# Performance work log

Measured on AMD Instinct MI355X. Metric: run time of the kernel, lower is better.

Reference implementation:

```python
import jax, jax.numpy as jnp
import numpy as np

EMBED = 32; HEADS = 4; HD = 8; FFN = 64; OBS = 64; CTX = 128; BATCH = 16
INIT_SCALE = 1.0 / np.sqrt(2.0 * 5.0)  # 1/sqrt(2*(3 spatial + 2 temporal))


def rmsnorm(x, w, eps=1e-6):
    return x / jnp.sqrt(jnp.mean(x * x, axis=-1, keepdims=True) + eps) * w


def rope_cache(T):
    theta = 1.0 / (10000.0 ** (jnp.arange(0, HD, 2, dtype=jnp.float32) / HD))
    freqs = jnp.arange(T, dtype=jnp.float32)[:, None] * theta[None, :]  # [T, HD//2]
    return jnp.cos(freqs), jnp.sin(freqs)


def apply_rope(x, cos, sin):
    half = x.shape[-1] // 2
    x1, x2 = x[..., :half], x[..., half:]
    c, s = cos[None, None], sin[None, None]  # broadcast over [B, H, T, HD//2]
    return jnp.concatenate([x1 * c - x2 * s, x2 * c + x1 * s], axis=-1)


def attn_block(x, Wq, Wk, Wv, Wo, Wg, Wval, Wout, norm4, qkn, cos=None, sin=None):
    B, S, W = x.shape
    h = rmsnorm(x, norm4[0])

    def proj(Wm):
        return jnp.einsum('bsw,dw->bsd', h, Wm).reshape(B, S, HEADS, HD).transpose(0, 2, 1, 3)

    q = rmsnorm(proj(Wq), qkn[0])
    k = rmsnorm(proj(Wk), qkn[1])
    v = proj(Wv)
    if cos is not None:
        q = apply_rope(q, cos, sin)
        k = apply_rope(k, cos, sin)
    scores = jnp.einsum('bhqd,bhkd->bhqk', q, k) / np.float32(np.sqrt(HD))
    o = jnp.einsum('bhqk,bhkd->bhqd', jax.nn.softmax(scores, axis=-1), v)
    o = o.transpose(0, 2, 1, 3).reshape(B, S, W)
    x = x + rmsnorm(jnp.einsum('bsw,dw->bsd', o, Wo), norm4[1])
    h2 = rmsnorm(x, norm4[2])
    ffn = jax.nn.silu(jnp.einsum('bsw,fw->bsf', h2, Wg)) * jnp.einsum('bsw,fw->bsf', h2, Wval)
    x = x + rmsnorm(jnp.einsum('bsf,wf->bsw', ffn, Wout), norm4[3])
    return x


def setup_inputs():
    key = jax.random.key(0)
    ks = iter(jax.random.split(key, 40))
    sd = 1.0 / np.sqrt(EMBED)
    inp = {
        'obs_seq': jax.random.normal(next(ks), (BATCH, CTX, OBS), jnp.float32),
        'W_val': jax.random.normal(next(ks), (EMBED, 1), jnp.float32),
        'b_val': jnp.zeros((EMBED,), jnp.float32),
        'input_norm_w': jnp.ones((EMBED,), jnp.float32),
        'dim_embed': jax.random.normal(next(ks), (OBS, EMBED), jnp.float32),
        'cls_tokens': jax.random.normal(next(ks), (3, EMBED), jnp.float32) * sd,
        'final_norm_w': jnp.ones((EMBED,), jnp.float32),
    }
    for pre, n in (('s', 3), ('t', 2)):
        inp[pre + '_Wq'] = jax.random.normal(next(ks), (n, EMBED, EMBED), jnp.float32) * sd
        inp[pre + '_Wk'] = jax.random.normal(next(ks), (n, EMBED, EMBED), jnp.float32) * sd
        inp[pre + '_Wv'] = jax.random.normal(next(ks), (n, EMBED, EMBED), jnp.float32) * sd
        inp[pre + '_Wo'] = jax.random.normal(next(ks), (n, EMBED, EMBED), jnp.float32) * (0.1 * INIT_SCALE * sd)
        inp[pre + '_Wg'] = jax.random.normal(next(ks), (n, FFN, EMBED), jnp.float32) * sd
        inp[pre + '_Wval'] = jax.random.normal(next(ks), (n, FFN, EMBED), jnp.float32) * sd
        inp[pre + '_Wout'] = jax.random.normal(next(ks), (n, EMBED, FFN), jnp.float32) * (INIT_SCALE / np.sqrt(FFN))
        inp[pre + '_norm4'] = jnp.ones((n, 4, EMBED), jnp.float32)
        inp[pre + '_qkn'] = jnp.ones((n, 2, HD), jnp.float32)
    return inp


def reference(obs_seq, W_val, b_val, input_norm_w, dim_embed, cls_tokens, final_norm_w,
              s_Wq, s_Wk, s_Wv, s_Wo, s_Wg, s_Wval, s_Wout, s_norm4, s_qkn,
              t_Wq, t_Wk, t_Wv, t_Wo, t_Wg, t_Wval, t_Wout, t_norm4, t_qkn):
    B, T, D = obs_seq.shape
    slots = D + 3
    # value_proj: Linear(1, EMBED) applied to each scalar feature
    tok = obs_seq[..., None] * W_val[:, 0] + b_val            # [B, T, D, EMBED]
    tok = tok + dim_embed[None, None]                          # dim id embedding
    cls = jnp.broadcast_to(cls_tokens[None, None], (B, T, 3, EMBED))
    tokens = rmsnorm(jnp.concatenate([tok, cls], axis=2), input_norm_w)  # [B,T,slots,EMBED]
    cos, sin = rope_cache(T)

    def spatial(tk, i):
        x = tk.reshape(B * T, slots, EMBED)
        x = attn_block(x, s_Wq[i], s_Wk[i], s_Wv[i], s_Wo[i], s_Wg[i], s_Wval[i], s_Wout[i], s_norm4[i], s_qkn[i])
        return x.reshape(B, T, slots, EMBED)

    def temporal(tk, i):
        x = tk.transpose(0, 2, 1, 3).reshape(B * slots, T, EMBED)
        x = attn_block(x, t_Wq[i], t_Wk[i], t_Wv[i], t_Wo[i], t_Wg[i], t_Wval[i], t_Wout[i], t_norm4[i], t_qkn[i], cos, sin)
        return x.reshape(B, slots, T, EMBED).transpose(0, 2, 1, 3)

    tokens = spatial(tokens, 0)
    tokens = temporal(tokens, 0)
    tokens = spatial(tokens, 1)
    tokens = temporal(tokens, 1)
    tokens = spatial(tokens, 2)
    tokens = rmsnorm(tokens, final_norm_w)
    last = tokens[:, -1]  # [B, slots, EMBED]
    return last[:, D], last[:, D + 1], last[:, D + 2]
```

## Files before the change

kernel.cpp:

```cpp
#include <hip/hip_runtime.h>

#define B_ 16
#define T_ 128
#define OBS_ 64
#define SLOTS_ 67
#define E_ 32
#define H_ 4
#define HD_ 8
#define FFN_ 64

typedef _Float16 h2 __attribute__((ext_vector_type(2)));
typedef _Float16 h4 __attribute__((ext_vector_type(4)));
typedef _Float16 h8 __attribute__((ext_vector_type(8)));
typedef __fp16 mh4 __attribute__((ext_vector_type(4)));
typedef __fp16 mh8 __attribute__((ext_vector_type(8)));
typedef float fx4 __attribute__((ext_vector_type(4)));
union H4u { h4 v; h2 h[2]; };

#define WBLK 10240
#define X16_BYTES (B_ * T_ * SLOTS_ * E_ * 2)
#define W16_BYTES (5 * WBLK * 2)
#define ROPE_OFF (X16_BYTES + W16_BYTES)
#define EMBED_BLOCKS ((B_ * T_ * SLOTS_ + 7) / 8)

__device__ __forceinline__ float red32(float v) {
  v += __shfl_xor(v, 16); v += __shfl_xor(v, 8); v += __shfl_xor(v, 4);
  v += __shfl_xor(v, 2);  v += __shfl_xor(v, 1);
  return v;
}
__device__ __forceinline__ float red8(float v) {
  v += __shfl_xor(v, 4); v += __shfl_xor(v, 2); v += __shfl_xor(v, 1);
  return v;
}
__device__ __forceinline__ float bfly16(float v) {
  v += __shfl_xor(v, 1); v += __shfl_xor(v, 2);
  v += __shfl_xor(v, 4); v += __shfl_xor(v, 8);
  return v;
}
__device__ __forceinline__ h2 pkrtz(float x, float y) {
  return __builtin_bit_cast(h2, __builtin_amdgcn_cvt_pkrtz(x, y));
}
__device__ __forceinline__ float rcp_(float x) { return __builtin_amdgcn_rcpf(x); }
__device__ __forceinline__ float rsq_(float x) { return __builtin_amdgcn_rsqf(x); }
__device__ __forceinline__ fx4 mfma16(h8 a, h8 b, fx4 c) {
  return __builtin_amdgcn_mfma_f32_16x16x32_f16(
      __builtin_bit_cast(mh8, a), __builtin_bit_cast(mh8, b), c, 0, 0, 0);
}
__device__ __forceinline__ fx4 mfma16k16(h4 a, h4 b, fx4 c) {
  return __builtin_amdgcn_mfma_f32_16x16x16f16(
      __builtin_bit_cast(mh4, a), __builtin_bit_cast(mh4, b), c, 0, 0, 0);
}

struct WPtrs {
  const float *sWq, *sWk, *sWv, *sWo, *sWg, *sWvl, *sWout;
  const float *tWq, *tWk, *tWv, *tWo, *tWg, *tWvl, *tWout;
};

#define CVT_BLOCKS 100

__global__ __launch_bounds__(256) void setup_kernel(
    WPtrs p, _Float16* __restrict__ dst,
    const float* __restrict__ obs, const float* __restrict__ Wval,
    const float* __restrict__ bval, const float* __restrict__ innw,
    const float* __restrict__ dimemb, const float* __restrict__ cls,
    float2* __restrict__ rope, _Float16* __restrict__ X) {
  if (blockIdx.x < CVT_BLOCKS) {
    int i = blockIdx.x * 256 + threadIdx.x;
    const int total_pairs = 5 * WBLK / 2;
    if (i >= total_pairs) return;
    int blk = i / (WBLK / 2);
    int f = (i % (WBLK / 2)) * 2;
    bool sp = blk < 3;
    int bi = sp ? blk : blk - 3;
    const float* src;
    int o;
    if (f < 1024)      { src = (sp ? p.sWq : p.tWq) + bi * 1024;  o = f; }
    else if (f < 2048) { src = (sp ? p.sWk : p.tWk) + bi * 1024;  o = f - 1024; }
    else if (f < 3072) { src = (sp ? p.sWv : p.tWv) + bi * 1024;  o = f - 2048; }
    else if (f < 4096) { src = (sp ? p.sWo : p.tWo) + bi * 1024;  o = f - 3072; }
    else if (f < 6144) { src = (sp ? p.sWg : p.tWg) + bi * 2048;  o = f - 4096; }
    else if (f < 8192) { src = (sp ? p.sWvl : p.tWvl) + bi * 2048; o = f - 6144; }
    else               { src = (sp ? p.sWout : p.tWout) + bi * 2048; o = f - 8192; }
    ((h2*)dst)[i] = pkrtz(src[o], src[o + 1]);
  } else if (blockIdx.x < CVT_BLOCKS + EMBED_BLOCKS) {
    int tok = (blockIdx.x - CVT_BLOCKS) * 8 + (threadIdx.x >> 5);
    int e = threadIdx.x & 31;
    const int total = B_ * T_ * SLOTS_;
    if (tok >= total) return;
    int slot = tok % SLOTS_;
    int bt = tok / SLOTS_;
    float v;
    if (slot < OBS_) {
      float o = obs[bt * OBS_ + slot];
      v = o * Wval[e] + bval[e] + dimemb[slot * E_ + e];
    } else {
      v = cls[(slot - OBS_) * E_ + e];
    }
    float ss = red32(v * v);
    X[tok * E_ + e] = (_Float16)(v * rsq_(ss * (1.0f / E_) + 1e-6f) * innw[e]);
  } else {
    for (int i = threadIdx.x; i < T_ * 4; i += 256) {
      int pos = i >> 2, j = i & 3;
      float th = __builtin_amdgcn_exp2f(-(float)j * 3.3219280948873623f);
      float sv, cv;
      __sincosf((float)pos * th, &sv, &cv);
      rope[i] = make_float2(cv, sv);
    }
  }
}

template <int SV, int SP, bool TEMPORAL, bool LAST>
__device__ __forceinline__ void block_body(
    _Float16* __restrict__ X, const _Float16* __restrict__ W16,
    const float* __restrict__ norm4, const float* __restrict__ qkn,
    const float2* __restrict__ rope, const float* __restrict__ fnw,
    float* __restrict__ out, int bid) {
  constexpr int MT = SP / 16;
  constexpr int MTW = (MT + 3) / 4;
  constexpr int VSTRIDE = TEMPORAL ? 128 : 168;
  constexpr int VROWS = TEMPORAL ? 32 : 33;
  __shared__ __align__(16) _Float16 smem[SP * 96 + VROWS * VSTRIDE];
  _Float16* hb = smem;
  _Float16* qb = smem + SP * 32;
  _Float16* kb = smem + SP * 64;
  _Float16* vT = smem + SP * 96;
  _Float16* ffnb = qb;

  const int tid = threadIdx.x;
  const int l = tid & 63, wv = tid >> 6;
  const int lm = l & 15, lq = l >> 4, hd = l & 7;

  auto vt_idx = [](int d, int s) {
    if (TEMPORAL) return d * 128 + (((s & ~15) ^ ((d & 7) << 4)) | (s & 15));
    return d * VSTRIDE + s;
  };

  int base, stride;
  if (TEMPORAL) {
    int b = bid / SLOTS_;
    int slot = bid % SLOTS_;
    base = (b * T_ * SLOTS_ + slot) * E_;
    stride = SLOTS_ * E_;
  } else {
    base = bid * 2 * SLOTS_ * E_;
    stride = E_;
  }

  const float nw0a = norm4[lm],      nw0b = norm4[16 + lm];
  const float nw1a = norm4[32 + lm], nw1b = norm4[48 + lm];
  const float nw2a = norm4[64 + lm], nw2b = norm4[80 + lm];
  const float nw3a = norm4[96 + lm], nw3b = norm4[112 + lm];
  const fx4 fz = {0.f, 0.f, 0.f, 0.f};
  const float qw = qkn[hd], kw = qkn[8 + hd];
  const float qscale = 0.35355339059327373f * 1.4426950408889634f;

  float xr[MTW][4][2];
#pragma unroll
  for (int t = 0; t < MTW; t++) {
    int mt = wv + 4 * t;
    if (mt < MT) {
#pragma unroll
      for (int r = 0; r < 4; r++) {
        int s = mt * 16 + lq * 4 + r;
        bool ok = (SV == SP) || (s < SV);
        int off = base + s * stride;
        xr[t][r][0] = ok ? (float)X[off + lm] : 0.f;
        xr[t][r][1] = ok ? (float)X[off + 16 + lm] : 0.f;
      }
    }
  }
#pragma unroll
  for (int t = 0; t < MTW; t++) {
    int mt = wv + 4 * t;
    if (mt < MT) {
#pragma unroll
      for (int r = 0; r < 4; r++) {
        int s = mt * 16 + lq * 4 + r;
        float p = bfly16(xr[t][r][0] * xr[t][r][0] + xr[t][r][1] * xr[t][r][1]);
        float inv = rsq_(p * (1.0f / E_) + 1e-6f);
        if (SV == SP || s < SV) {
          hb[s * 32 + lm] = (_Float16)(xr[t][r][0] * inv * nw0a);
          hb[s * 32 + 16 + lm] = (_Float16)(xr[t][r][1] * inv * nw0b);
        }
      }
    }
  }
  __syncthreads();

  for (int u = wv; u < MT * 2; u += 4) {
    const int mt = u >> 1, nt = u & 1;
    h8 aH = *(const h8*)(hb + (mt * 16 + lm) * 32 + lq * 8);
    float rc[4], rs[4];
    if (TEMPORAL) {
#pragma unroll
      for (int r = 0; r < 4; r++) {
        float2 cs = rope[(mt * 16 + lq * 4 + r) * 4 + (hd & 3)];
        rc[r] = cs.x; rs[r] = cs.y;
      }
    }
    const int d = nt * 16 + lm;
    h8 bq = *(const h8*)(W16 + (nt * 16 + lm) * 32 + lq * 8);
    h8 bk = *(const h8*)(W16 + 1024 + (nt * 16 + lm) * 32 + lq * 8);
    h8 bv = *(const h8*)(W16 + 2048 + (nt * 16 + lm) * 32 + lq * 8);
    fx4 aq = mfma16(aH, bq, fz);
    fx4 ak = mfma16(aH, bk, fz);
    fx4 av = mfma16(aH, bv, fz);
#pragma unroll
    for (int r = 0; r < 4; r++) {
      int s = mt * 16 + lq * 4 + r;
      float q1 = aq[r], k1 = ak[r];
      float qv = q1 * rsq_(red8(q1 * q1) * 0.125f + 1e-6f) * qw;
      float kv = k1 * rsq_(red8(k1 * k1) * 0.125f + 1e-6f) * kw;
      if (TEMPORAL) {
        float qp = __shfl_xor(qv, 4);
        float kp = __shfl_xor(kv, 4);
        qv = (hd < 4) ? (qv * rc[r] - qp * rs[r]) : (qv * rc[r] + qp * rs[r]);
        kv = (hd < 4) ? (kv * rc[r] - kp * rs[r]) : (kv * rc[r] + kp * rs[r]);
      }
      if (SV == SP || s < SV) {
        qb[s * 32 + d] = (_Float16)(qv * qscale);
        kb[s * 32 + d] = (_Float16)kv;
      }
    }
    const int s0 = mt * 16 + lq * 4;
    const int va = vt_idx(d, s0);
    if (SV == SP || s0 + 1 < SV) *(h2*)(vT + va) = pkrtz(av[0], av[1]);
    if (SV == SP || s0 + 3 < SV) *(h2*)(vT + va + 2) = pkrtz(av[2], av[3]);
  }
  if (!TEMPORAL) {
    for (int idx = tid; idx < 32 * 13; idx += 256) {
      int d = idx / 13, c = 2 * SLOTS_ + 2 * (idx % 13);
      *(h2*)(vT + d * VSTRIDE + c) = pkrtz(0.f, 0.f);
    }
    for (int idx = tid; idx < VSTRIDE / 2; idx += 256) {
      *(h2*)(vT + 32 * VSTRIDE + 2 * idx) = pkrtz(1.f, 1.f);
    }
  }
  __syncthreads();

  {
    const int h = wv;
    const h8 z8 = {};
    const h4 ones4 = {(_Float16)1.f, (_Float16)1.f, (_Float16)1.f, (_Float16)1.f};
    const bool vlane = (lm < 8);
    const int dv = h * 8 + (lm & 7);
    const int vrow = (!TEMPORAL && !vlane) ? 32 : dv;
    for (int mt = 0; mt < MT; mt++) {
      h8 bQ = *(const h8*)(qb + (mt * 16 + lm) * 32 + lq * 8);
      bQ = (lq == h) ? bQ : z8;
      const int q = mt * 16 + lm;
      fx4 oaccT = fz;

      auto ktile = [&](int kt, int mode) {
        h8 aK = *(const h8*)(kb + (kt * 16 + lm) * 32 + lq * 8);
        fx4 sc = mfma16(aK, bQ, fz);
        float ev[4];
#pragma unroll
        for (int r = 0; r < 4; r++) {
          float x = __builtin_amdgcn_exp2f(sc[r]);
          int kidx = kt * 16 + lq * 4 + r;
          if (mode == 1) x = (kidx < SLOTS_) ? x : 0.f;
          else if (mode == 2) x = (kidx >= SLOTS_) ? x : 0.f;
          else if (mode == 3) x = (kidx < 2 * SLOTS_) ? x : 0.f;
          else if (mode == 4) {
            bool ok = (kidx < 2 * SLOTS_) && ((kidx < SLOTS_) == (q < SLOTS_));
            x = ok ? x : 0.f;
          }
          ev[r] = x;
        }
        H4u pT;
        pT.h[0] = pkrtz(ev[0], ev[1]);
        pT.h[1] = pkrtz(ev[2], ev[3]);
        h4 aV = *(const h4*)(vT + vt_idx(vrow, kt * 16 + lq * 4));
        if (TEMPORAL) aV = vlane ? aV : ones4;
        oaccT = mfma16k16(aV, pT.v, oaccT);
      };

      if (TEMPORAL) {
#pragma unroll
        for (int kt = 0; kt < SP / 16; kt++) ktile(kt, 0);
      } else if (mt <= 3) {
#pragma unroll
        for (int kt = 0; kt < 4; kt++) ktile(kt, 0);
        ktile(4, 1);
      } else if (mt == 4) {
#pragma unroll
        for (int kt = 0; kt < MT; kt++) ktile(kt, 4);
      } else {
        ktile(4, 2);
#pragma unroll
        for (int kt = 5; kt < 8; kt++) ktile(kt, 0);
        ktile(8, 3);
      }

      float lsum = __shfl_xor(oaccT[0], 32);
      float inv = rcp_(lsum);
      if (lq < 2 && (SV == SP || q < SV)) {
        H4u ov;
        ov.h[0] = pkrtz(oaccT[0] * inv, oaccT[1] * inv);
        ov.h[1] = pkrtz(oaccT[2] * inv, oaccT[3] * inv);
        *(h4*)(hb + q * 32 + h * 8 + lq * 4) = ov.v;
      }
    }
  }
  __syncthreads();

#pragma unroll
  for (int t = 0; t < MTW; t++) {
    int mt = wv + 4 * t;
    if (mt < MT) {
      h8 aO = *(const h8*)(hb + (mt * 16 + lm) * 32 + lq * 8);
      h8 b0 = *(const h8*)(W16 + 3072 + lm * 32 + lq * 8);
      h8 b1 = *(const h8*)(W16 + 3072 + (16 + lm) * 32 + lq * 8);
      fx4 a0 = mfma16(aO, b0, fz);
      fx4 a1 = mfma16(aO, b1, fz);
#pragma unroll
      for (int r = 0; r < 4; r++) {
        int s = mt * 16 + lq * 4 + r;
        float p = bfly16(a0[r] * a0[r] + a1[r] * a1[r]);
        float inv = rsq_(p * (1.0f / E_) + 1e-6f);
        xr[t][r][0] += a0[r] * inv * nw1a;
        xr[t][r][1] += a1[r] * inv * nw1b;
        float q2 = bfly16(xr[t][r][0] * xr[t][r][0] + xr[t][r][1] * xr[t][r][1]);
        float inv2 = rsq_(q2 * (1.0f / E_) + 1e-6f);
        if (SV == SP || s < SV) {
          hb[s * 32 + lm] = (_Float16)(xr[t][r][0] * inv2 * nw2a);
          hb[s * 32 + 16 + lm] = (_Float16)(xr[t][r][1] * inv2 * nw2b);
        }
      }
    }
  }
  __syncthreads();

  for (int u = wv; u < MT * 4; u += 4) {
    const int mt = u >> 2, nt = u & 3;
    h8 aH2 = *(const h8*)(hb + (mt * 16 + lm) * 32 + lq * 8);
    h8 bg = *(const h8*)(W16 + 4096 + (nt * 16 + lm) * 32 + lq * 8);
    h8 bl = *(const h8*)(W16 + 6144 + (nt * 16 + lm) * 32 + lq * 8);
    fx4 g = mfma16(aH2, bg, fz);
    fx4 vvv = mfma16(aH2, bl, fz);
#pragma unroll
    for (int r = 0; r < 4; r++) {
      int s = mt * 16 + lq * 4 + r;
      if (SV == SP || s < SV) {
        float gg = g[r];
        float sg = gg * rcp_(1.0f + __builtin_amdgcn_exp2f(gg * -1.4426950408889634f));
        ffnb[s * 64 + nt * 16 + lm] = (_Float16)(sg * vvv[r]);
      }
    }
  }
  __syncthreads();

#pragma unroll
  for (int t = 0; t < MTW; t++) {
    int mt = wv + 4 * t;
    if (mt < MT) {
      const _Float16* fr = ffnb + (mt * 16 + lm) * 64;
      h8 a0 = *(const h8*)(fr + lq * 8);
      h8 a1 = *(const h8*)(fr + 32 + lq * 8);
      h8 b00 = *(const h8*)(W16 + 8192 + lm * 64 + lq * 8);
      h8 b01 = *(const h8*)(W16 + 8192 + lm * 64 + 32 + lq * 8);
      h8 b10 = *(const h8*)(W16 + 8192 + (16 + lm) * 64 + lq * 8);
      h8 b11 = *(const h8*)(W16 + 8192 + (16 + lm) * 64 + 32 + lq * 8);
      fx4 o0 = mfma16(a1, b01, mfma16(a0, b00, fz));
      fx4 o1 = mfma16(a1, b11, mfma16(a0, b10, fz));
#pragma unroll
      for (int r = 0; r < 4; r++) {
        int s = mt * 16 + lq * 4 + r;
        float p = bfly16(o0[r] * o0[r] + o1[r] * o1[r]);
        float inv = rsq_(p * (1.0f / E_) + 1e-6f);
        xr[t][r][0] += o0[r] * inv * nw3a;
        xr[t][r][1] += o1[r] * inv * nw3b;
        if (SV == SP || s < SV) {
          int off = base + s * stride;
          X[off + lm] = (_Float16)xr[t][r][0];
          X[off + 16 + lm] = (_Float16)xr[t][r][1];
        }
      }
      if (LAST && mt == MT - 1 && (bid & (T_ / 2 - 1)) == (T_ / 2 - 1)) {
        const int b = bid / (T_ / 2);
#pragma unroll
        for (int r = 0; r < 4; r++) {
          int s = mt * 16 + lq * 4 + r;
          int j = s - (SLOTS_ + OBS_);
          float p2 = bfly16(xr[t][r][0] * xr[t][r][0] + xr[t][r][1] * xr[t][r][1]);
          if (j >= 0 && j < 3) {
            float inv2 = rsq_(p2 * (1.0f / E_) + 1e-6f);
            out[j * (B_ * E_) + b * E_ + lm] = xr[t][r][0] * inv2 * fnw[lm];
            out[j * (B_ * E_) + b * E_ + 16 + lm] = xr[t][r][1] * inv2 * fnw[16 + lm];
          }
        }
      }
    }
  }
}

__global__ __launch_bounds__(256, 4) void attn_spatial_kernel(
    _Float16* __restrict__ X, const _Float16* __restrict__ W16,
    const float* __restrict__ norm4, const float* __restrict__ qkn) {
  block_body<2 * SLOTS_, 144, false, false>(X, W16, norm4, qkn, nullptr,
                                            nullptr, nullptr, blockIdx.x);
}

__global__ __launch_bounds__(256, 4) void attn_spatial_last_kernel(
    _Float16* __restrict__ X, const _Float16* __restrict__ W16,
    const float* __restrict__ norm4, const float* __restrict__ qkn,
    const float* __restrict__ fnw, float* __restrict__ out) {
  block_body<2 * SLOTS_, 144, false, true>(X, W16, norm4, qkn, nullptr,
                                           fnw, out, blockIdx.x);
}

__global__ __launch_bounds__(256, 5) void attn_temporal_kernel(
    _Float16* __restrict__ X, const _Float16* __restrict__ W16,
    const float* __restrict__ norm4, const float* __restrict__ qkn,
    const float2* __restrict__ rope) {
  block_body<T_, 128, true, false>(X, W16, norm4, qkn, rope,
                                   nullptr, nullptr, blockIdx.x);
}

extern "C" void kernel_launch(void* const* d_in, const int* in_sizes, int n_in,
                              void* d_out, int out_size, void* d_ws, size_t ws_size,
                              hipStream_t stream) {
  (void)in_sizes; (void)n_in; (void)out_size; (void)ws_size;
  const float* obs          = (const float*)d_in[0];
  const float* W_val        = (const float*)d_in[1];
  const float* b_val        = (const float*)d_in[2];
  const float* input_norm_w = (const float*)d_in[3];
  const float* dim_embed    = (const float*)d_in[4];
  const float* cls_tokens   = (const float*)d_in[5];
  const float* final_norm_w = (const float*)d_in[6];
  const float* s_n4   = (const float*)d_in[14];
  const float* s_qkn  = (const float*)d_in[15];
  const float* t_n4   = (const float*)d_in[23];
  const float* t_qkn  = (const float*)d_in[24];

  _Float16* X = (_Float16*)d_ws;
  _Float16* W16 = (_Float16*)((char*)d_ws + X16_BYTES);
  float2* rope = (float2*)((char*)d_ws + ROPE_OFF);
  float* out = (float*)d_out;

  WPtrs wp;
  wp.sWq   = (const float*)d_in[7];
  wp.sWk   = (const float*)d_in[8];
  wp.sWv   = (const float*)d_in[9];
  wp.sWo   = (const float*)d_in[10];
  wp.sWg   = (const float*)d_in[11];
  wp.sWvl  = (const float*)d_in[12];
  wp.sWout = (const float*)d_in[13];
  wp.tWq   = (const float*)d_in[16];
  wp.tWk   = (const float*)d_in[17];
  wp.tWv   = (const float*)d_in[18];
  wp.tWo   = (const float*)d_in[19];
  wp.tWg   = (const float*)d_in[20];
  wp.tWvl  = (const float*)d_in[21];
  wp.tWout = (const float*)d_in[22];

  setup_kernel<<<CVT_BLOCKS + EMBED_BLOCKS + 1, 256, 0, stream>>>(
      wp, W16, obs, W_val, b_val, input_norm_w, dim_embed, cls_tokens, rope, X);

  const int N4 = 4 * E_;
  const int QN = 2 * HD_;

#define SPATIAL(i)                                                     \
  attn_spatial_kernel<<<B_ * T_ / 2, 256, 0, stream>>>(                \
      X, W16 + (i)*WBLK, s_n4 + (i)*N4, s_qkn + (i)*QN)
#define TEMPORAL(i)                                                    \
  attn_temporal_kernel<<<B_ * SLOTS_, 256, 0, stream>>>(               \
      X, W16 + (3 + (i)) * WBLK, t_n4 + (i)*N4, t_qkn + (i)*QN, rope)

  SPATIAL(0);
  TEMPORAL(0);
  SPATIAL(1);
  TEMPORAL(1);
  attn_spatial_last_kernel<<<B_ * T_ / 2, 256, 0, stream>>>(
      X, W16 + 2 * WBLK, s_n4 + 2 * N4, s_qkn + 2 * QN, final_norm_w, out);

#undef SPATIAL
#undef TEMPORAL
}
```

Before: 310.4 us.

## Swizzle LDS buffers, pair query tiles in attention, batch embed tokens per block

Adds XOR-swizzled shared-memory indexing for the hb/qb/kb (32-wide) and ffnb (64-wide) buffers to reduce LDS bank conflicts on the h8 row loads. Restructures the attention loop so each K tile load and V load serves two query tiles at once, with two independent MFMA chains for more instruction-level parallelism. Makes the setup embedding blocks process 64 tokens each instead of 8. The costs are higher register pressure from the paired accumulators and extra index arithmetic; EMBED_BLOCKS now relies on the token count dividing evenly by 64.

```diff
diff --git a/kernel.cpp b/kernel.cpp
--- a/kernel.cpp
+++ b/kernel.cpp
@@ -21,7 +21,7 @@
 #define X16_BYTES (B_ * T_ * SLOTS_ * E_ * 2)
 #define W16_BYTES (5 * WBLK * 2)
 #define ROPE_OFF (X16_BYTES + W16_BYTES)
-#define EMBED_BLOCKS ((B_ * T_ * SLOTS_ + 7) / 8)
+#define EMBED_BLOCKS (B_ * T_ * SLOTS_ / 64)
 
 __device__ __forceinline__ float red32(float v) {
   v += __shfl_xor(v, 16); v += __shfl_xor(v, 8); v += __shfl_xor(v, 4);
@@ -49,6 +49,13 @@
 __device__ __forceinline__ fx4 mfma16k16(h4 a, h4 b, fx4 c) {
   return __builtin_amdgcn_mfma_f32_16x16x16f16(
       __builtin_bit_cast(mh4, a), __builtin_bit_cast(mh4, b), c, 0, 0, 0);
+}
+
+__device__ __forceinline__ int sw32(int row, int col) {
+  return row * 32 + (col ^ (((row >> 1) & 3) << 3));
+}
+__device__ __forceinline__ int sw64(int row, int col) {
+  return row * 64 + (col ^ ((row & 7) << 3));
 }
 
 struct WPtrs {
@@ -83,21 +90,23 @@
     else               { src = (sp ? p.sWout : p.tWout) + bi * 2048; o = f - 8192; }
     ((h2*)dst)[i] = pkrtz(src[o], src[o + 1]);
   } else if (blockIdx.x < CVT_BLOCKS + EMBED_BLOCKS) {
-    int tok = (blockIdx.x - CVT_BLOCKS) * 8 + (threadIdx.x >> 5);
+    int t0 = (blockIdx.x - CVT_BLOCKS) * 64 + (threadIdx.x >> 5);
     int e = threadIdx.x & 31;
-    const int total = B_ * T_ * SLOTS_;
-    if (tok >= total) return;
-    int slot = tok % SLOTS_;
-    int bt = tok / SLOTS_;
-    float v;
-    if (slot < OBS_) {
-      float o = obs[bt * OBS_ + slot];
-      v = o * Wval[e] + bval[e] + dimemb[slot * E_ + e];
-    } else {
-      v = cls[(slot - OBS_) * E_ + e];
-    }
-    float ss = red32(v * v);
-    X[tok * E_ + e] = (_Float16)(v * rsq_(ss * (1.0f / E_) + 1e-6f) * innw[e]);
+#pragma unroll
+    for (int i = 0; i < 8; i++) {
+      int tok = t0 + i * 8;
+      int slot = tok % SLOTS_;
+      int bt = tok / SLOTS_;
+      float v;
+      if (slot < OBS_) {
+        float o = obs[bt * OBS_ + slot];
+        v = o * Wval[e] + bval[e] + dimemb[slot * E_ + e];
+      } else {
+        v = cls[(slot - OBS_) * E_ + e];
+      }
+      float ss = red32(v * v);
+      X[tok * E_ + e] = (_Float16)(v * rsq_(ss * (1.0f / E_) + 1e-6f) * innw[e]);
+    }
   } else {
     for (int i = threadIdx.x; i < T_ * 4; i += 256) {
       int pos = i >> 2, j = i & 3;
@@ -179,8 +188,8 @@
         float p = bfly16(xr[t][r][0] * xr[t][r][0] + xr[t][r][1] * xr[t][r][1]);
         float inv = rsq_(p * (1.0f / E_) + 1e-6f);
         if (SV == SP || s < SV) {
-          hb[s * 32 + lm] = (_Float16)(xr[t][r][0] * inv * nw0a);
-          hb[s * 32 + 16 + lm] = (_Float16)(xr[t][r][1] * inv * nw0b);
+          hb[sw32(s, lm)] = (_Float16)(xr[t][r][0] * inv * nw0a);
+          hb[sw32(s, 16 + lm)] = (_Float16)(xr[t][r][1] * inv * nw0b);
         }
       }
     }
@@ -189,7 +198,7 @@
 
   for (int u = wv; u < MT * 2; u += 4) {
     const int mt = u >> 1, nt = u & 1;
-    h8 aH = *(const h8*)(hb + (mt * 16 + lm) * 32 + lq * 8);
+    h8 aH = *(const h8*)(hb + sw32(mt * 16 + lm, lq * 8));
     float rc[4], rs[4];
     if (TEMPORAL) {
 #pragma unroll
@@ -218,8 +227,8 @@
         kv = (hd < 4) ? (kv * rc[r] - kp * rs[r]) : (kv * rc[r] + kp * rs[r]);
       }
       if (SV == SP || s < SV) {
-        qb[s * 32 + d] = (_Float16)(qv * qscale);
-        kb[s * 32 + d] = (_Float16)kv;
+        qb[sw32(s, d)] = (_Float16)(qv * qscale);
+        kb[sw32(s, d)] = (_Float16)kv;
       }
     }
     const int s0 = mt * 16 + lq * 4;
@@ -245,61 +254,105 @@
     const bool vlane = (lm < 8);
     const int dv = h * 8 + (lm & 7);
     const int vrow = (!TEMPORAL && !vlane) ? 32 : dv;
-    for (int mt = 0; mt < MT; mt++) {
-      h8 bQ = *(const h8*)(qb + (mt * 16 + lm) * 32 + lq * 8);
-      bQ = (lq == h) ? bQ : z8;
-      const int q = mt * 16 + lm;
-      fx4 oaccT = fz;
-
-      auto ktile = [&](int kt, int mode) {
-        h8 aK = *(const h8*)(kb + (kt * 16 + lm) * 32 + lq * 8);
-        fx4 sc = mfma16(aK, bQ, fz);
-        float ev[4];
-#pragma unroll
-        for (int r = 0; r < 4; r++) {
-          float x = __builtin_amdgcn_exp2f(sc[r]);
-          int kidx = kt * 16 + lq * 4 + r;
-          if (mode == 1) x = (kidx < SLOTS_) ? x : 0.f;
-          else if (mode == 2) x = (kidx >= SLOTS_) ? x : 0.f;
-          else if (mode == 3) x = (kidx < 2 * SLOTS_) ? x : 0.f;
-          else if (mode == 4) {
-            bool ok = (kidx < 2 * SLOTS_) && ((kidx < SLOTS_) == (q < SLOTS_));
-            x = ok ? x : 0.f;
-          }
-          ev[r] = x;
-        }
-        H4u pT;
-        pT.h[0] = pkrtz(ev[0], ev[1]);
-        pT.h[1] = pkrtz(ev[2], ev[3]);
-        h4 aV = *(const h4*)(vT + vt_idx(vrow, kt * 16 + lq * 4));
-        if (TEMPORAL) aV = vlane ? aV : ones4;
-        oaccT = mfma16k16(aV, pT.v, oaccT);
-      };
-
-      if (TEMPORAL) {
-#pragma unroll
-        for (int kt = 0; kt < SP / 16; kt++) ktile(kt, 0);
-      } else if (mt <= 3) {
-#pragma unroll
-        for (int kt = 0; kt < 4; kt++) ktile(kt, 0);
-        ktile(4, 1);
-      } else if (mt == 4) {
-#pragma unroll
-        for (int kt = 0; kt < MT; kt++) ktile(kt, 4);
-      } else {
-        ktile(4, 2);
-#pragma unroll
-        for (int kt = 5; kt < 8; kt++) ktile(kt, 0);
-        ktile(8, 3);
-      }
-
-      float lsum = __shfl_xor(oaccT[0], 32);
+
+    auto loadQ = [&](int mt) {
+      h8 b = *(const h8*)(qb + sw32(mt * 16 + lm, lq * 8));
+      return (lq == h) ? b : z8;
+    };
+    auto maskx = [&](float x, int kidx, int mode, int q) {
+      if (mode == 1) return (kidx < SLOTS_) ? x : 0.f;
+      if (mode == 2) return (kidx >= SLOTS_) ? x : 0.f;
+      if (mode == 3) return (kidx < 2 * SLOTS_) ? x : 0.f;
+      if (mode == 4) {
+        bool ok = (kidx < 2 * SLOTS_) && ((kidx < SLOTS_) == (q < SLOTS_));
+        return ok ? x : 0.f;
+      }
+      return x;
+    };
+    auto ktile2 = [&](int kt, int mode, const h8& bQ0, const h8& bQ1,
+                      fx4& o0, fx4& o1) {
+      h8 aK = *(const h8*)(kb + sw32(kt * 16 + lm, lq * 8));
+      fx4 s0 = mfma16(aK, bQ0, fz);
+      fx4 s1 = mfma16(aK, bQ1, fz);
+      float e0[4], e1[4];
+#pragma unroll
+      for (int r = 0; r < 4; r++) {
+        int kidx = kt * 16 + lq * 4 + r;
+        e0[r] = maskx(__builtin_amdgcn_exp2f(s0[r]), kidx, mode, 0);
+        e1[r] = maskx(__builtin_amdgcn_exp2f(s1[r]), kidx, mode, 0);
+      }
+      H4u p0, p1;
+      p0.h[0] = pkrtz(e0[0], e0[1]); p0.h[1] = pkrtz(e0[2], e0[3]);
+      p1.h[0] = pkrtz(e1[0], e1[1]); p1.h[1] = pkrtz(e1[2], e1[3]);
+      h4 aV = *(const h4*)(vT + vt_idx(vrow, kt * 16 + lq * 4));
+      if (TEMPORAL) aV = vlane ? aV : ones4;
+      o0 = mfma16k16(aV, p0.v, o0);
+      o1 = mfma16k16(aV, p1.v, o1);
+    };
+    auto ktile1 = [&](int kt, int mode, int q, const h8& bQ, fx4& oa) {
+      h8 aK = *(const h8*)(kb + sw32(kt * 16 + lm, lq * 8));
+      fx4 sc = mfma16(aK, bQ, fz);
+      float ev[4];
+#pragma unroll
+      for (int r = 0; r < 4; r++) {
+        int kidx = kt * 16 + lq * 4 + r;
+        ev[r] = maskx(__builtin_amdgcn_exp2f(sc[r]), kidx, mode, q);
+      }
+      H4u pT;
+      pT.h[0] = pkrtz(ev[0], ev[1]); pT.h[1] = pkrtz(ev[2], ev[3]);
+      h4 aV = *(const h4*)(vT + vt_idx(vrow, kt * 16 + lq * 4));
+      if (TEMPORAL) aV = vlane ? aV : ones4;
+      oa = mfma16k16(aV, pT.v, oa);
+    };
+    auto finish = [&](int mt, fx4& oa) {
+      int q = mt * 16 + lm;
+      float lsum = __shfl_xor(oa[0], 32);
       float inv = rcp_(lsum);
       if (lq < 2 && (SV == SP || q < SV)) {
         H4u ov;
-        ov.h[0] = pkrtz(oaccT[0] * inv, oaccT[1] * inv);
-        ov.h[1] = pkrtz(oaccT[2] * inv, oaccT[3] * inv);
-        *(h4*)(hb + q * 32 + h * 8 + lq * 4) = ov.v;
+        ov.h[0] = pkrtz(oa[0] * inv, oa[1] * inv);
+        ov.h[1] = pkrtz(oa[2] * inv, oa[3] * inv);
+        *(h4*)(hb + sw32(q, h * 8 + lq * 4)) = ov.v;
+      }
+    };
+
+    if (TEMPORAL) {
+      for (int mtp = 0; mtp < MT / 2; mtp++) {
+        h8 bQ0 = loadQ(2 * mtp), bQ1 = loadQ(2 * mtp + 1);
+        fx4 o0 = fz, o1 = fz;
+#pragma unroll
+        for (int kt = 0; kt < MT; kt++) ktile2(kt, 0, bQ0, bQ1, o0, o1);
+        finish(2 * mtp, o0);
+        finish(2 * mtp + 1, o1);
+      }
+    } else {
+      for (int mtp = 0; mtp < 2; mtp++) {
+        h8 bQ0 = loadQ(2 * mtp), bQ1 = loadQ(2 * mtp + 1);
+        fx4 o0 = fz, o1 = fz;
+#pragma unroll
+        for (int kt = 0; kt < 4; kt++) ktile2(kt, 0, bQ0, bQ1, o0, o1);
+        ktile2(4, 1, bQ0, bQ1, o0, o1);
+        finish(2 * mtp, o0);
+        finish(2 * mtp + 1, o1);
+      }
+      {
+        h8 bQ = loadQ(4);
+        fx4 oa = fz;
+        const int q = 4 * 16 + lm;
+#pragma unroll
+        for (int kt = 0; kt < MT; kt++) ktile1(kt, 4, q, bQ, oa);
+        finish(4, oa);
+      }
+      for (int mtp = 0; mtp < 2; mtp++) {
+        int m0 = 5 + 2 * mtp;
+        h8 bQ0 = loadQ(m0), bQ1 = loadQ(m0 + 1);
+        fx4 o0 = fz, o1 = fz;
+        ktile2(4, 2, bQ0, bQ1, o0, o1);
+#pragma unroll
+        for (int kt = 5; kt < 8; kt++) ktile2(kt, 0, bQ0, bQ1, o0, o1);
+        ktile2(8, 3, bQ0, bQ1, o0, o1);
+        finish(m0, o0);
+        finish(m0 + 1, o1);
       }
     }
   }
@@ -309,7 +362,7 @@
   for (int t = 0; t < MTW; t++) {
     int mt = wv + 4 * t;
     if (mt < MT) {
-      h8 aO = *(const h8*)(hb + (mt * 16 + lm) * 32 + lq * 8);
+      h8 aO = *(const h8*)(hb + sw32(mt * 16 + lm, lq * 8));
       h8 b0 = *(const h8*)(W16 + 3072 + lm * 32 + lq * 8);
       h8 b1 = *(const h8*)(W16 + 3072 + (16 + lm) * 32 + lq * 8);
       fx4 a0 = mfma16(aO, b0, fz);
@@ -324,8 +377,8 @@
         float q2 = bfly16(xr[t][r][0] * xr[t][r][0] + xr[t][r][1] * xr[t][r][1]);
         float inv2 = rsq_(q2 * (1.0f / E_) + 1e-6f);
         if (SV == SP || s < SV) {
-          hb[s * 32 + lm] = (_Float16)(xr[t][r][0] * inv2 * nw2a);
-          hb[s * 32 + 16 + lm] = (_Float16)(xr[t][r][1] * inv2 * nw2b);
+          hb[sw32(s, lm)] = (_Float16)(xr[t][r][0] * inv2 * nw2a);
+          hb[sw32(s, 16 + lm)] = (_Float16)(xr[t][r][1] * inv2 * nw2b);
         }
       }
     }
@@ -334,7 +387,7 @@
 
   for (int u = wv; u < MT * 4; u += 4) {
     const int mt = u >> 2, nt = u & 3;
-    h8 aH2 = *(const h8*)(hb + (mt * 16 + lm) * 32 + lq * 8);
+    h8 aH2 = *(const h8*)(hb + sw32(mt * 16 + lm, lq * 8));
     h8 bg = *(const h8*)(W16 + 4096 + (nt * 16 + lm) * 32 + lq * 8);
     h8 bl = *(const h8*)(W16 + 6144 + (nt * 16 + lm) * 32 + lq * 8);
     fx4 g = mfma16(aH2, bg, fz);
@@ -345,7 +398,7 @@
       if (SV == SP || s < SV) {
         float gg = g[r];
         float sg = gg * rcp_(1.0f + __builtin_amdgcn_exp2f(gg * -1.4426950408889634f));
-        ffnb[s * 64 + nt * 16 + lm] = (_Float16)(sg * vvv[r]);
+        ffnb[sw64(s, nt * 16 + lm)] = (_Float16)(sg * vvv[r]);
       }
     }
   }
@@ -355,9 +408,9 @@
   for (int t = 0; t < MTW; t++) {
     int mt = wv + 4 * t;
     if (mt < MT) {
-      const _Float16* fr = ffnb + (mt * 16 + lm) * 64;
-      h8 a0 = *(const h8*)(fr + lq * 8);
-      h8 a1 = *(const h8*)(fr + 32 + lq * 8);
+      const int row = mt * 16 + lm;
+      h8 a0 = *(const h8*)(ffnb + sw64(row, lq * 8));
+      h8 a1 = *(const h8*)(ffnb + sw64(row, 32 + lq * 8));
       h8 b00 = *(const h8*)(W16 + 8192 + lm * 64 + lq * 8);
       h8 b01 = *(const h8*)(W16 + 8192 + lm * 64 + 32 + lq * 8);
       h8 b10 = *(const h8*)(W16 + 8192 + (16 + lm) * 64 + lq * 8);
```

New measurement: 312.3 us. About the same (+0.6%).
